# Performance work log

Measured on AMD Instinct MI355X. Metric: run time of the kernel, lower is better.

The kernel has to match this reference:

```python
import jax, jax.numpy as jnp
import numpy as np

WL_W = 8   # weight quantization bits (args.wl_weight)
WL_A = 8   # activation quantization bits (args.wl_activate)
EPS = 1e-5


def _quant_ste(x, bits):
    """Symmetric per-tensor uniform quantization with straight-through estimator,
    emulating NeuroSim's wage-style weight/activation quantization in QConv2d."""
    n = float(2 ** (bits - 1) - 1)
    s = jnp.max(jnp.abs(x)) + 1e-12
    xq = jnp.round(x / s * n) / n * s
    return x + jax.lax.stop_gradient(xq - x)


def _qconv(x, w):
    # quantize input and weight, then 3x3 conv, stride 1, padding 1 (NCHW/OIHW)
    xq = _quant_ste(x, WL_A)
    wq = _quant_ste(w, WL_W)
    return jax.lax.conv_general_dilated(
        xq, wq, window_strides=(1, 1), padding=((1, 1), (1, 1)),
        dimension_numbers=('NCHW', 'OIHW', 'NCHW'))


def _bn(x, gamma, beta):
    # training-mode BatchNorm2d: batch statistics over (N, H, W)
    mean = jnp.mean(x, axis=(0, 2, 3), keepdims=True)
    var = jnp.var(x, axis=(0, 2, 3), keepdims=True)
    xn = (x - mean) * jax.lax.rsqrt(var + EPS)
    return xn * gamma[None, :, None, None] + beta[None, :, None, None]


def setup_inputs() -> dict:
    key = jax.random.key(0)
    ks = jax.random.split(key, 3)
    B, C, H, W = 32, 128, 56, 56
    return {
        'x': jax.random.normal(ks[0], (B, C, H, W), dtype=jnp.float32),
        'w1': jax.random.normal(ks[1], (C, C, 3, 3), dtype=jnp.float32) * 0.05,
        'gamma1': jnp.ones((C,), dtype=jnp.float32),
        'beta1': jnp.zeros((C,), dtype=jnp.float32),
        'w2': jax.random.normal(ks[2], (C, C, 3, 3), dtype=jnp.float32) * 0.05,
        'gamma2': jnp.ones((C,), dtype=jnp.float32),
        'beta2': jnp.zeros((C,), dtype=jnp.float32),
    }


def reference(x, w1, gamma1, beta1, w2, gamma2, beta2):
    identity = x  # no downsample
    out = _qconv(x, w1)
    out = _bn(out, gamma1, beta1)
    out = jax.nn.relu(out)
    out = _qconv(out, w2)
    out = _bn(out, gamma2, beta2)
    out = out + identity
    return jax.nn.relu(out)
```

## Files before the change

kernel.cpp:

```cpp
#include <hip/hip_runtime.h>

#define NB 32
#define C 128
#define H 56
#define W 56
#define HWSZ (H*W)
#define ELTS (NB*C*HWSZ)
#define NHW (NB*HWSZ)
#define HP 59
#define SLAB 8192
#define GCONVX 28
#define NBLK (GCONVX*NB)
#define NBLK2 (NBLK*2)

typedef __attribute__((ext_vector_type(8))) short bf16x8;
typedef __attribute__((ext_vector_type(4))) short short4v;
typedef __attribute__((ext_vector_type(4))) float f32x4;
typedef __attribute__((ext_vector_type(4))) int i32x4;

#define SLOT_SX 0
#define SLOT_SW1 1
#define SLOT_SW2 2
#define SLOT_SA2 3
#define SUM1 8
#define SSQ1 136
#define MAXE1 264
#define MAXNEG1 392
#define SCALE1 520
#define SHIFT1 648
#define SUM2 776
#define SSQ2 904
#define MAXE2 1032
#define MAXNEG2 1160
#define SCALE2 1288
#define SHIFT2 1416

#define META_OFF 0ull
#define META_BYTES 8192ull
#define XQ_OFF 8192ull
#define XQ_BYTES ((unsigned long long)NB*HP*SLAB)
#define A2Q_OFF (XQ_OFF + XQ_BYTES)
#define Y1_OFF (A2Q_OFF + XQ_BYTES)
#define Y_BYTES ((unsigned long long)ELTS*2ull)
#define Y2_OFF (Y1_OFF + Y_BYTES)
#define W1Q_OFF (Y2_OFF + Y_BYTES)
#define WQ_BYTES (9ull*2*128*64)
#define W2Q_OFF (W1Q_OFF + WQ_BYTES)
#define PART_OFF (W2Q_OFF + WQ_BYTES)
#define PART_BYTES ((unsigned long long)NBLK2*512*4)

__device__ __forceinline__ short f2bf_rne(float f) {
    unsigned u = __float_as_uint(f);
    return (short)((u + 0x7FFFu + ((u >> 16) & 1u)) >> 16);
}
__device__ __forceinline__ float bf2f(short s) {
    return __uint_as_float(((unsigned)(unsigned short)s) << 16);
}
__device__ __forceinline__ unsigned fenc(float f) {
    unsigned u = __float_as_uint(f);
    return (u & 0x80000000u) ? ~u : (u | 0x80000000u);
}
__device__ __forceinline__ float fdec(unsigned e) {
    unsigned u = (e & 0x80000000u) ? (e ^ 0x80000000u) : ~e;
    return __uint_as_float(u);
}

__global__ void absmax_kernel(const float* __restrict__ p, int n4, unsigned* __restrict__ slot) {
    __shared__ float red[256];
    float m = 0.f;
    int stride = gridDim.x * blockDim.x;
    for (int i = blockIdx.x * blockDim.x + threadIdx.x; i < n4; i += stride) {
        f32x4 v = ((const f32x4*)p)[i];
        m = fmaxf(m, fmaxf(fmaxf(fabsf(v.x), fabsf(v.y)), fmaxf(fabsf(v.z), fabsf(v.w))));
    }
    red[threadIdx.x] = m;
    __syncthreads();
    for (int s = 128; s > 0; s >>= 1) {
        if (threadIdx.x < s) red[threadIdx.x] = fmaxf(red[threadIdx.x], red[threadIdx.x + s]);
        __syncthreads();
    }
    if (threadIdx.x == 0) atomicMax(slot, __float_as_uint(red[0]));
}

__global__ void absmax_w_kernel(const float* __restrict__ w1, const float* __restrict__ w2,
                                unsigned* __restrict__ metau) {
    __shared__ float red[256];
    const float* p = blockIdx.y ? w2 : w1;
    unsigned* slot = metau + (blockIdx.y ? SLOT_SW2 : SLOT_SW1);
    const int n4 = 147456 / 4;
    float m = 0.f;
    int stride = gridDim.x * blockDim.x;
    for (int i = blockIdx.x * blockDim.x + threadIdx.x; i < n4; i += stride) {
        f32x4 v = ((const f32x4*)p)[i];
        m = fmaxf(m, fmaxf(fmaxf(fabsf(v.x), fabsf(v.y)), fmaxf(fabsf(v.z), fabsf(v.w))));
    }
    red[threadIdx.x] = m;
    __syncthreads();
    for (int s = 128; s > 0; s >>= 1) {
        if (threadIdx.x < s) red[threadIdx.x] = fmaxf(red[threadIdx.x], red[threadIdx.x + s]);
        __syncthreads();
    }
    if (threadIdx.x == 0) atomicMax(slot, __float_as_uint(red[0]));
}

__global__ void pad_zero_kernel(char* __restrict__ xq, char* __restrict__ a2q,
                                float* __restrict__ meta) {
    int hp = blockIdx.x;
    int n = blockIdx.y;
    char* base = (blockIdx.z ? a2q : xq) + ((size_t)n * HP + hp) * SLAB;
    int t = threadIdx.x;
    if (blockIdx.z == 0 && blockIdx.x == 0 && blockIdx.y == 0) {
        #pragma unroll
        for (int j = 0; j < 8; ++j) meta[j * 256 + t] = 0.f;
    }
    if (hp == 0 || hp >= 57) {
        f32x4 z = {0.f, 0.f, 0.f, 0.f};
        *(f32x4*)(base + t * 16) = z;
        *(f32x4*)(base + 4096 + t * 16) = z;
    } else {
        if (t < 32) *(int*)(base + t * 4) = 0;
        else        *(int*)(base + 7296 + (t - 32) * 4) = 0;
    }
}

__global__ void quant_w_kernel(const float* __restrict__ w1, const float* __restrict__ w2,
                               const float* __restrict__ meta,
                               char* __restrict__ w1q, char* __restrict__ w2q) {
    const float* w = blockIdx.y ? w2 : w1;
    char* wq = blockIdx.y ? w2q : w1q;
    float qs = 127.f / (meta[blockIdx.y ? SLOT_SW2 : SLOT_SW1] + 1e-12f);
    int idx = blockIdx.x * 256 + threadIdx.x;
    int co = idx >> 7, ci = idx & 127;
    const float* src = w + ((size_t)(co * 128 + ci)) * 9;
    int cc = ci >> 6, cl = ci & 63;
    #pragma unroll
    for (int tap = 0; tap < 9; ++tap) {
        int q = (int)rintf(src[tap] * qs);
        wq[(((size_t)tap * 2 + cc) * 128 + co) * 64 + cl] = (char)q;
    }
}

__global__ void quant_x_kernel(const float* __restrict__ x, const float* __restrict__ meta,
                               char* __restrict__ xq) {
    __shared__ float tile[128][57];
    int h = blockIdx.x, n = blockIdx.y, t = threadIdx.x;
    int ci = t >> 1, seg = (t & 1) * 28;
    const float* row = x + (((size_t)(n * C + ci)) * H + h) * W + seg;
    #pragma unroll
    for (int j = 0; j < 28; j += 4) {
        f32x4 v = *(const f32x4*)(row + j);
        tile[ci][seg + j + 0] = v.x;
        tile[ci][seg + j + 1] = v.y;
        tile[ci][seg + j + 2] = v.z;
        tile[ci][seg + j + 3] = v.w;
    }
    __syncthreads();
    float qs = 127.f / (meta[SLOT_SX] + 1e-12f);
    int w = t & 63, cq = t >> 6;
    if (w < 56) {
        char* slab = xq + ((size_t)n * HP + (h + 1)) * SLAB;
        int wp = w + 1;
        #pragma unroll
        for (int c2 = 0; c2 < 2; ++c2) {
            union { char c[16]; i32x4 v; } u;
            #pragma unroll
            for (int j = 0; j < 16; ++j)
                u.c[j] = (char)(int)rintf(tile[cq * 32 + c2 * 16 + j][w] * qs);
            int L = wp * 128 + cq * 32 + c2 * 16;
            *(i32x4*)(slab + (L ^ ((wp & 7) << 4))) = u.v;
        }
    }
}

__global__ __launch_bounds__(256, 4) void conv_mfma_kernel(
        const char* __restrict__ xq, const char* __restrict__ wq,
        short* __restrict__ y, const float* __restrict__ meta,
        float* __restrict__ part, int slot_in, int slot_w) {
    __shared__ __align__(16) char lds[4 * SLAB + 512];
    const int n = blockIdx.y, h0 = blockIdx.x * 2;
    const int t = threadIdx.x, lane = t & 63;
    const int wv = t >> 6, r = wv >> 1, ch = (wv & 1) * 64;
    const int l15 = lane & 15, lg = lane >> 4;

    const char* slabbase = xq + ((size_t)n * HP + h0) * SLAB;
    #pragma unroll
    for (int s = 0; s < 4; ++s) {
        #pragma unroll
        for (int i = 0; i < 2; ++i) {
            int off = (i * 256 + t) * 16;
            __builtin_amdgcn_global_load_lds(
                (const __attribute__((address_space(1))) unsigned*)(slabbase + s * SLAB + off),
                (__attribute__((address_space(3))) unsigned*)(lds + s * SLAB + off), 16, 0, 0);
        }
    }

    i32x4 acc[4][4] = {};

    #pragma unroll
    for (int kh = 0; kh < 3; ++kh) {
        if (kh == 0)      { asm volatile("s_waitcnt vmcnt(4)" ::: "memory"); }
        else if (kh == 1) { asm volatile("s_waitcnt vmcnt(2)" ::: "memory"); }
        else              { asm volatile("s_waitcnt vmcnt(0)" ::: "memory"); }
        __builtin_amdgcn_s_barrier();
        const char* Bb = lds + (kh + r) * SLAB;
        #pragma unroll
        for (int kw = 0; kw < 3; ++kw) {
            #pragma unroll
            for (int cc = 0; cc < 2; ++cc) {
                const char* wt = wq + (((kh * 3 + kw) * 2 + cc) << 13);
                i32x4 a[4];
                #pragma unroll
                for (int ct = 0; ct < 4; ++ct)
                    a[ct] = *(const i32x4*)(wt + (ch + ct * 16 + l15) * 64 + lg * 16);
                #pragma unroll
                for (int fj = 0; fj < 4; ++fj) {
                    int wpp = fj * 16 + l15 + kw;
                    int L = (wpp << 7) + (cc << 6) + (lg << 4);
                    i32x4 b = *(const i32x4*)(Bb + (L ^ ((wpp & 7) << 4)));
                    #pragma unroll
                    for (int ct = 0; ct < 4; ++ct)
                        acc[ct][fj] = __builtin_amdgcn_mfma_i32_16x16x64_i8(a[ct], b, acc[ct][fj], 0, 0, 0);
                }
            }
        }
    }

    float dq = (meta[slot_in] + 1e-12f) * (meta[slot_w] + 1e-12f) * (1.f / 16129.f);

    __syncthreads();
    char* ylds = lds;
    float* slds = (float*)(lds + 28672);

    #pragma unroll
    for (int ct = 0; ct < 4; ++ct) {
        float s1[4] = {}, s2[4] = {}, m1[4], m2[4];
        #pragma unroll
        for (int q = 0; q < 4; ++q) { m1[q] = -1e30f; m2[q] = -1e30f; }
        #pragma unroll
        for (int fj = 0; fj < 4; ++fj) {
            int wo = fj * 16 + l15;
            if (wo < W) {
                short4v pk;
                #pragma unroll
                for (int q = 0; q < 4; ++q) {
                    float v = (float)acc[ct][fj][q] * dq;
                    s1[q] += v;
                    s2[q] += v * v;
                    m1[q] = fmaxf(m1[q], v);
                    m2[q] = fmaxf(m2[q], -v);
                    pk[q] = f2bf_rne(v);
                }
                int a = r * 14336 + wo * 256 + ch * 2 + ct * 32 + lg * 8;
                *(short4v*)(ylds + (a ^ ((wo & 7) << 4))) = pk;
            }
        }
        #pragma unroll
        for (int q = 0; q < 4; ++q) {
            #pragma unroll
            for (int m = 1; m < 16; m <<= 1) {
                s1[q] += __shfl_xor(s1[q], m, 64);
                s2[q] += __shfl_xor(s2[q], m, 64);
                m1[q] = fmaxf(m1[q], __shfl_xor(m1[q], m, 64));
                m2[q] = fmaxf(m2[q], __shfl_xor(m2[q], m, 64));
            }
        }
        if (l15 == 0) {
            #pragma unroll
            for (int q = 0; q < 4; ++q) {
                int c = ch + ct * 16 + lg * 4 + q;
                slds[r * 512 + 0 * 128 + c] = s1[q];
                slds[r * 512 + 1 * 128 + c] = s2[q];
                slds[r * 512 + 2 * 128 + c] = m1[q];
                slds[r * 512 + 3 * 128 + c] = m2[q];
            }
        }
    }
    __syncthreads();

    short* ybase = y + (((size_t)n * H + h0) * W) * C;
    #pragma unroll
    for (int i = 0; i < 7; ++i) {
        int g = i * 256 + t;
        int r2 = g >= 896;
        int rem = g - r2 * 896;
        int wo = rem >> 4, cb = rem & 15;
        int a = r2 * 14336 + wo * 256 + cb * 16;
        bf16x8 v = *(const bf16x8*)(ylds + (a ^ ((wo & 7) << 4)));
        *(bf16x8*)(ybase + ((size_t)r2 * W + wo) * C + cb * 8) = v;
    }

    {
        int bh = t >> 7;
        int off = t & 127;
        int p = off >> 5, cs = (off & 31) * 4;
        f32x4 sv = *(const f32x4*)(slds + bh * 512 + p * 128 + cs);
        size_t bcol = (size_t)(blockIdx.y * GCONVX + blockIdx.x) * 2 + bh;
        *(f32x4*)(part + bcol * 512 + p * 128 + cs) = sv;
    }
}

__global__ void bn_reduce_kernel(const float* __restrict__ part, float* __restrict__ meta,
                                 int sum_off, int ssq_off, int maxe_off, int maxneg_off) {
    int t = threadIdx.x, b = blockIdx.x;
    const float* base = part + (size_t)b * 28 * 512;
    float vadd = 0.f, vmax = -1e30f;
    for (int i = 0; i < 28; ++i) {
        vadd += base[i * 512 + t];
        vmax = fmaxf(vmax, base[i * 512 + 256 + t]);
    }
    int c = t & 127;
    unsigned* metau = (unsigned*)meta;
    if (t < 128) {
        atomicAdd(&meta[sum_off + c], vadd);
        atomicMax(metau + maxe_off + c, fenc(vmax));
    } else {
        atomicAdd(&meta[ssq_off + c], vadd);
        atomicMax(metau + maxneg_off + c, fenc(vmax));
    }
}

__global__ void bn_finalize_kernel(float* __restrict__ meta, int sum_off, int ssq_off,
                                   int maxe_off, int maxneg_off, int scale_off, int shift_off,
                                   int amax_slot,
                                   const float* __restrict__ gamma, const float* __restrict__ beta) {
    __shared__ float red[128];
    int c = threadIdx.x;
    float mean = meta[sum_off + c] * (1.f / NHW);
    float var = meta[ssq_off + c] * (1.f / NHW) - mean * mean;
    float istd = rsqrtf(var + 1e-5f);
    float sc = gamma[c] * istd;
    float sh = beta[c] - mean * sc;
    meta[scale_off + c] = sc;
    meta[shift_off + c] = sh;
    if (amax_slot >= 0) {
        float vmax = fdec(((unsigned*)meta)[maxe_off + c]);
        float vmin = -fdec(((unsigned*)meta)[maxneg_off + c]);
        float cand = fmaxf(0.f, fmaxf(sc * vmax + sh, sc * vmin + sh));
        red[c] = cand;
        __syncthreads();
        for (int k = 64; k > 0; k >>= 1) {
            if (c < k) red[c] = fmaxf(red[c], red[c + k]);
            __syncthreads();
        }
        if (c == 0) meta[amax_slot] = red[0];
    }
}

__global__ void quant_bnrelu_kernel(const short* __restrict__ y1, const float* __restrict__ meta,
                                    char* __restrict__ a2q) {
    int h = blockIdx.x, n = blockIdx.y, t = threadIdx.x;
    const short* row = y1 + (((size_t)n * H + h) * W) * C;
    float qs = 127.f / (meta[SLOT_SA2] + 1e-12f);
    char* slab = a2q + ((size_t)n * HP + (h + 1)) * SLAB;
    #pragma unroll
    for (int i = 0; i < 2; ++i) {
        int g = i * 256 + t;
        if (g < 448) {
            int w = g >> 3, cg = g & 7;
            bf16x8 v0 = *(const bf16x8*)(row + w * 128 + cg * 16);
            bf16x8 v1 = *(const bf16x8*)(row + w * 128 + cg * 16 + 8);
            union { char c[16]; i32x4 v; } u;
            #pragma unroll
            for (int j = 0; j < 8; ++j) {
                float a = fmaxf(bf2f(v0[j]) * meta[SCALE1 + cg * 16 + j] + meta[SHIFT1 + cg * 16 + j], 0.f);
                u.c[j] = (char)(int)rintf(a * qs);
            }
            #pragma unroll
            for (int j = 0; j < 8; ++j) {
                float a = fmaxf(bf2f(v1[j]) * meta[SCALE1 + cg * 16 + 8 + j] + meta[SHIFT1 + cg * 16 + 8 + j], 0.f);
                u.c[8 + j] = (char)(int)rintf(a * qs);
            }
            int wp = w + 1;
            int L = wp * 128 + cg * 16;
            *(i32x4*)(slab + (L ^ ((wp & 7) << 4))) = u.v;
        }
    }
}

__global__ void final_kernel(const short* __restrict__ y2, const float* __restrict__ x,
                             const float* __restrict__ meta, float* __restrict__ out) {
    __shared__ short tile[56 * 128];
    int h = blockIdx.x, n = blockIdx.y, t = threadIdx.x;
    const short* row = y2 + (((size_t)n * H + h) * W) * C;
    #pragma unroll
    for (int i = 0; i < 4; ++i) {
        int g = i * 256 + t;
        if (g < 896) *(bf16x8*)(tile + g * 8) = *(const bf16x8*)(row + g * 8);
    }
    __syncthreads();
    int c = t >> 1, seg = (t & 1) * 28;
    float sc = meta[SCALE2 + c], sh = meta[SHIFT2 + c];
    const float* xr = x + (((size_t)(n * C + c)) * H + h) * W + seg;
    float* orow = out + (((size_t)(n * C + c)) * H + h) * W + seg;
    #pragma unroll
    for (int j = 0; j < 28; j += 4) {
        f32x4 xv = *(const f32x4*)(xr + j);
        f32x4 o;
        #pragma unroll
        for (int k = 0; k < 4; ++k) {
            float yv = bf2f(tile[(seg + j + k) * 128 + c]);
            o[k] = fmaxf(yv * sc + sh + xv[k], 0.f);
        }
        *(f32x4*)(orow + j) = o;
    }
}

extern "C" void kernel_launch(void* const* d_in, const int* in_sizes, int n_in,
                              void* d_out, int out_size, void* d_ws, size_t ws_size,
                              hipStream_t stream) {
    const float* x      = (const float*)d_in[0];
    const float* w1     = (const float*)d_in[1];
    const float* gamma1 = (const float*)d_in[2];
    const float* beta1  = (const float*)d_in[3];
    const float* w2     = (const float*)d_in[4];
    const float* gamma2 = (const float*)d_in[5];
    const float* beta2  = (const float*)d_in[6];
    float* out = (float*)d_out;
    char* ws = (char*)d_ws;

    float* meta = (float*)(ws + META_OFF);
    unsigned* metau = (unsigned*)meta;
    char* xq   = ws + XQ_OFF;
    char* a2q  = ws + A2Q_OFF;
    short* y1  = (short*)(ws + Y1_OFF);
    short* y2  = (short*)(ws + Y2_OFF);
    char* w1q  = ws + W1Q_OFF;
    char* w2q  = ws + W2Q_OFF;
    float* part = (float*)(ws + PART_OFF);

    pad_zero_kernel<<<dim3(59, 32, 2), 256, 0, stream>>>(xq, a2q, meta);

    absmax_kernel<<<1024, 256, 0, stream>>>(x, ELTS / 4, metau + SLOT_SX);
    absmax_w_kernel<<<dim3(64, 2), 256, 0, stream>>>(w1, w2, metau);
    quant_w_kernel<<<dim3(64, 2), 256, 0, stream>>>(w1, w2, meta, w1q, w2q);

    dim3 ghn(56, 32);
    quant_x_kernel<<<ghn, 256, 0, stream>>>(x, meta, xq);

    dim3 gconv(GCONVX, 32);
    conv_mfma_kernel<<<gconv, 256, 0, stream>>>(xq, w1q, y1, meta, part, SLOT_SX, SLOT_SW1);
    bn_reduce_kernel<<<64, 256, 0, stream>>>(part, meta, SUM1, SSQ1, MAXE1, MAXNEG1);
    bn_finalize_kernel<<<1, 128, 0, stream>>>(meta, SUM1, SSQ1, MAXE1, MAXNEG1,
                                              SCALE1, SHIFT1, SLOT_SA2, gamma1, beta1);
    quant_bnrelu_kernel<<<ghn, 256, 0, stream>>>(y1, meta, a2q);

    conv_mfma_kernel<<<gconv, 256, 0, stream>>>(a2q, w2q, y2, meta, part, SLOT_SA2, SLOT_SW2);
    bn_reduce_kernel<<<64, 256, 0, stream>>>(part, meta, SUM2, SSQ2, MAXE2, MAXNEG2);
    bn_finalize_kernel<<<1, 128, 0, stream>>>(meta, SUM2, SSQ2, MAXE2, MAXNEG2,
                                              SCALE2, SHIFT2, -1, gamma2, beta2);

    final_kernel<<<ghn, 256, 0, stream>>>(y2, x, meta, out);
}
```

Measured before the change: 278.1 us.

## Compute one output row per conv block and store results directly to global

The int8 MFMA conv kernel now has each block handle a single output row. Its four waves each own 32 output channels, where before each wave covered 64 channels of one of two rows. This halves the accumulator registers and doubles the grid to 56x32 blocks, and the LDS staging pass for the bf16 output is dropped in favour of direct short4 global stores. The aim is better occupancy and less LDS traffic and synchronisation. The cost is that each block loads 3 input slabs for 1 row instead of 4 for 2, weight fragments are reloaded per row, and the output stores are less coalesced.

```diff
diff --git a/kernel.cpp b/kernel.cpp
--- a/kernel.cpp
+++ b/kernel.cpp
@@ -9,9 +9,7 @@
 #define NHW (NB*HWSZ)
 #define HP 59
 #define SLAB 8192
-#define GCONVX 28
-#define NBLK (GCONVX*NB)
-#define NBLK2 (NBLK*2)
+#define NBCOL (H*NB)
 
 typedef __attribute__((ext_vector_type(8))) short bf16x8;
 typedef __attribute__((ext_vector_type(4))) short short4v;
@@ -47,7 +45,7 @@
 #define WQ_BYTES (9ull*2*128*64)
 #define W2Q_OFF (W1Q_OFF + WQ_BYTES)
 #define PART_OFF (W2Q_OFF + WQ_BYTES)
-#define PART_BYTES ((unsigned long long)NBLK2*512*4)
+#define PART_BYTES ((unsigned long long)NBCOL*512*4)
 
 __device__ __forceinline__ short f2bf_rne(float f) {
     unsigned u = __float_as_uint(f);
@@ -176,15 +174,15 @@
         const char* __restrict__ xq, const char* __restrict__ wq,
         short* __restrict__ y, const float* __restrict__ meta,
         float* __restrict__ part, int slot_in, int slot_w) {
-    __shared__ __align__(16) char lds[4 * SLAB + 512];
-    const int n = blockIdx.y, h0 = blockIdx.x * 2;
+    __shared__ __align__(16) char lds[3 * SLAB + 512 + 2048];
+    const int n = blockIdx.y, h = blockIdx.x;
     const int t = threadIdx.x, lane = t & 63;
-    const int wv = t >> 6, r = wv >> 1, ch = (wv & 1) * 64;
+    const int co0 = (t >> 6) * 32;
     const int l15 = lane & 15, lg = lane >> 4;
 
-    const char* slabbase = xq + ((size_t)n * HP + h0) * SLAB;
-    #pragma unroll
-    for (int s = 0; s < 4; ++s) {
+    const char* slabbase = xq + ((size_t)n * HP + h) * SLAB;
+    #pragma unroll
+    for (int s = 0; s < 3; ++s) {
         #pragma unroll
         for (int i = 0; i < 2; ++i) {
             int off = (i * 256 + t) * 16;
@@ -194,7 +192,7 @@
         }
     }
 
-    i32x4 acc[4][4] = {};
+    i32x4 acc[2][4] = {};
 
     #pragma unroll
     for (int kh = 0; kh < 3; ++kh) {
@@ -202,23 +200,23 @@
         else if (kh == 1) { asm volatile("s_waitcnt vmcnt(2)" ::: "memory"); }
         else              { asm volatile("s_waitcnt vmcnt(0)" ::: "memory"); }
         __builtin_amdgcn_s_barrier();
-        const char* Bb = lds + (kh + r) * SLAB;
+        const char* Bb = lds + kh * SLAB;
         #pragma unroll
         for (int kw = 0; kw < 3; ++kw) {
             #pragma unroll
             for (int cc = 0; cc < 2; ++cc) {
                 const char* wt = wq + (((kh * 3 + kw) * 2 + cc) << 13);
-                i32x4 a[4];
+                i32x4 a[2];
                 #pragma unroll
-                for (int ct = 0; ct < 4; ++ct)
-                    a[ct] = *(const i32x4*)(wt + (ch + ct * 16 + l15) * 64 + lg * 16);
+                for (int ct = 0; ct < 2; ++ct)
+                    a[ct] = *(const i32x4*)(wt + (co0 + ct * 16 + l15) * 64 + lg * 16);
                 #pragma unroll
                 for (int fj = 0; fj < 4; ++fj) {
                     int wpp = fj * 16 + l15 + kw;
                     int L = (wpp << 7) + (cc << 6) + (lg << 4);
                     i32x4 b = *(const i32x4*)(Bb + (L ^ ((wpp & 7) << 4)));
                     #pragma unroll
-                    for (int ct = 0; ct < 4; ++ct)
+                    for (int ct = 0; ct < 2; ++ct)
                         acc[ct][fj] = __builtin_amdgcn_mfma_i32_16x16x64_i8(a[ct], b, acc[ct][fj], 0, 0, 0);
                 }
             }
@@ -226,13 +224,11 @@
     }
 
     float dq = (meta[slot_in] + 1e-12f) * (meta[slot_w] + 1e-12f) * (1.f / 16129.f);
-
-    __syncthreads();
-    char* ylds = lds;
-    float* slds = (float*)(lds + 28672);
-
-    #pragma unroll
-    for (int ct = 0; ct < 4; ++ct) {
+    short* yrow = y + (((size_t)n * H + h) * W) * C;
+    float* slds = (float*)(lds + 3 * SLAB + 512);
+
+    #pragma unroll
+    for (int ct = 0; ct < 2; ++ct) {
         float s1[4] = {}, s2[4] = {}, m1[4], m2[4];
         #pragma unroll
         for (int q = 0; q < 4; ++q) { m1[q] = -1e30f; m2[q] = -1e30f; }
@@ -250,8 +246,7 @@
                     m2[q] = fmaxf(m2[q], -v);
                     pk[q] = f2bf_rne(v);
                 }
-                int a = r * 14336 + wo * 256 + ch * 2 + ct * 32 + lg * 8;
-                *(short4v*)(ylds + (a ^ ((wo & 7) << 4))) = pk;
+                *(short4v*)(yrow + (size_t)wo * C + co0 + ct * 16 + lg * 4) = pk;
             }
         }
         #pragma unroll
@@ -267,34 +262,19 @@
         if (l15 == 0) {
             #pragma unroll
             for (int q = 0; q < 4; ++q) {
-                int c = ch + ct * 16 + lg * 4 + q;
-                slds[r * 512 + 0 * 128 + c] = s1[q];
-                slds[r * 512 + 1 * 128 + c] = s2[q];
-                slds[r * 512 + 2 * 128 + c] = m1[q];
-                slds[r * 512 + 3 * 128 + c] = m2[q];
+                int c = co0 + ct * 16 + lg * 4 + q;
+                slds[0 * 128 + c] = s1[q];
+                slds[1 * 128 + c] = s2[q];
+                slds[2 * 128 + c] = m1[q];
+                slds[3 * 128 + c] = m2[q];
             }
         }
     }
     __syncthreads();
-
-    short* ybase = y + (((size_t)n * H + h0) * W) * C;
-    #pragma unroll
-    for (int i = 0; i < 7; ++i) {
-        int g = i * 256 + t;
-        int r2 = g >= 896;
-        int rem = g - r2 * 896;
-        int wo = rem >> 4, cb = rem & 15;
-        int a = r2 * 14336 + wo * 256 + cb * 16;
-        bf16x8 v = *(const bf16x8*)(ylds + (a ^ ((wo & 7) << 4)));
-        *(bf16x8*)(ybase + ((size_t)r2 * W + wo) * C + cb * 8) = v;
-    }
-
-    {
-        int bh = t >> 7;
-        int off = t & 127;
-        int p = off >> 5, cs = (off & 31) * 4;
-        f32x4 sv = *(const f32x4*)(slds + bh * 512 + p * 128 + cs);
-        size_t bcol = (size_t)(blockIdx.y * GCONVX + blockIdx.x) * 2 + bh;
+    if (t < 128) {
+        int p = t >> 5, cs = (t & 31) * 4;
+        f32x4 sv = *(const f32x4*)(slds + p * 128 + cs);
+        size_t bcol = (size_t)n * H + h;
         *(f32x4*)(part + bcol * 512 + p * 128 + cs) = sv;
     }
 }
@@ -437,14 +417,13 @@
     dim3 ghn(56, 32);
     quant_x_kernel<<<ghn, 256, 0, stream>>>(x, meta, xq);
 
-    dim3 gconv(GCONVX, 32);
-    conv_mfma_kernel<<<gconv, 256, 0, stream>>>(xq, w1q, y1, meta, part, SLOT_SX, SLOT_SW1);
+    conv_mfma_kernel<<<ghn, 256, 0, stream>>>(xq, w1q, y1, meta, part, SLOT_SX, SLOT_SW1);
     bn_reduce_kernel<<<64, 256, 0, stream>>>(part, meta, SUM1, SSQ1, MAXE1, MAXNEG1);
     bn_finalize_kernel<<<1, 128, 0, stream>>>(meta, SUM1, SSQ1, MAXE1, MAXNEG1,
                                               SCALE1, SHIFT1, SLOT_SA2, gamma1, beta1);
     quant_bnrelu_kernel<<<ghn, 256, 0, stream>>>(y1, meta, a2q);
 
-    conv_mfma_kernel<<<gconv, 256, 0, stream>>>(a2q, w2q, y2, meta, part, SLOT_SA2, SLOT_SW2);
+    conv_mfma_kernel<<<ghn, 256, 0, stream>>>(a2q, w2q, y2, meta, part, SLOT_SA2, SLOT_SW2);
     bn_reduce_kernel<<<64, 256, 0, stream>>>(part, meta, SUM2, SSQ2, MAXE2, MAXNEG2);
     bn_finalize_kernel<<<1, 128, 0, stream>>>(meta, SUM2, SSQ2, MAXE2, MAXNEG2,
                                               SCALE2, SHIFT2, -1, gamma2, beta2);
```

Measured after the change: 251.5 us. -9.6%, faster.
